# Performance work log

Hardware: AMD Instinct MI355X
Metric: run time of the kernel (lower is better)

## Reference

```python
import jax, jax.numpy as jnp
import numpy as np

N_HEAD = 16
N_KV = 4
HEAD_DIM = 128
EPS = float(np.finfo(np.float32).eps)  # torch F.rms_norm default eps


def _rope_tables(T, half, dtype=jnp.float32):
    inv_freq = 1.0 / (10000.0 ** (jnp.arange(half, dtype=dtype) / half))
    ang = jnp.arange(T, dtype=dtype)[:, None] * inv_freq[None, :]  # (T, half)
    cos = jnp.cos(ang)[None, :, None, :]  # (1, T, 1, half)
    sin = jnp.sin(ang)[None, :, None, :]
    return cos, sin


def setup_inputs() -> dict:
    key = jax.random.key(0)
    ks = jax.random.split(key, 5)
    B, T, C = 2, 2048, 2048
    x = jax.random.normal(ks[0], (B, T, C), dtype=jnp.float32)
    cos, sin = _rope_tables(T, HEAD_DIM // 2)
    s = 0.02
    W_Q = jax.random.normal(ks[1], (C, N_HEAD * HEAD_DIM), dtype=jnp.float32) * s
    W_K = jax.random.normal(ks[2], (C, N_KV * HEAD_DIM), dtype=jnp.float32) * s
    W_V = jax.random.normal(ks[3], (C, N_KV * HEAD_DIM), dtype=jnp.float32) * s
    W_O = jax.random.normal(ks[4], (C, C), dtype=jnp.float32) * s
    return {"x": x, "cos": cos, "sin": sin, "W_Q": W_Q, "W_K": W_K, "W_V": W_V, "W_O": W_O}


def _apply_rope(x, cos, sin):
    # x: (B,T,H,D); cos/sin: (1,T,1,D/2)
    d = x.shape[-1] // 2
    x1, x2 = x[..., :d], x[..., d:]
    return jnp.concatenate([x1 * cos + x2 * sin, -x1 * sin + x2 * cos], axis=-1)


def _rms_norm(x):
    return x * jax.lax.rsqrt(jnp.mean(x * x, axis=-1, keepdims=True) + EPS)


def reference(x, cos, sin, W_Q, W_K, W_V, W_O):
    B, T, C = x.shape
    G = N_HEAD // N_KV  # kv groups
    q = (x @ W_Q).reshape(B, T, N_HEAD, HEAD_DIM)
    k = (x @ W_K).reshape(B, T, N_KV, HEAD_DIM)
    v = (x @ W_V).reshape(B, T, N_KV, HEAD_DIM)
    q = _rms_norm(_apply_rope(q, cos[:, :T], sin[:, :T]))
    k = _rms_norm(_apply_rope(k, cos[:, :T], sin[:, :T]))
    # GQA: avoid materializing expanded K/V; group q by kv head
    qg = q.reshape(B, T, N_KV, G, HEAD_DIM)
    scale = 1.0 / jnp.sqrt(jnp.asarray(HEAD_DIM, dtype=x.dtype))
    scores = jnp.einsum("btkgd,bskd->bkgts", qg, k) * scale  # (B,Kv,G,T,T)
    causal = jnp.tril(jnp.ones((T, T), dtype=bool))
    scores = jnp.where(causal, scores, jnp.asarray(-jnp.inf, dtype=scores.dtype))
    attn = jax.nn.softmax(scores, axis=-1)
    out = jnp.einsum("bkgts,bskd->btkgd", attn, v).reshape(B, T, C)
    return out @ W_O
```

## Files before the change

kernel.cpp:

```cpp
#include <hip/hip_runtime.h>
#include <hip/hip_bf16.h>
#include <stdint.h>

typedef __bf16 bf16_4 __attribute__((ext_vector_type(4)));
typedef __bf16 bf16_8 __attribute__((ext_vector_type(8)));
typedef float f32x4 __attribute__((ext_vector_type(4)));

#define AS1 __attribute__((address_space(1)))
#define AS3 __attribute__((address_space(3)))

__device__ __forceinline__ void gload_lds16(const void* g, void* l) {
  __builtin_amdgcn_global_load_lds((const AS1 void*)g, (AS3 void*)l, 16, 0, 0);
}

__global__ void detect_dtype(const void* __restrict__ cosT, int* __restrict__ flag) {
  uint32_t w = *reinterpret_cast<const uint32_t*>(cosT);
  *flag = ((w & 0xFFFFu) == 0x3F80u) ? 1 : 0;
}

__global__ __launch_bounds__(256) void to_bf16_vec(const void* __restrict__ src,
                                                   __bf16* __restrict__ dst,
                                                   int n8, const int* __restrict__ flag) {
  const int i = blockIdx.x * 256 + threadIdx.x;
  if (i >= n8) return;
  if (*flag) {
    reinterpret_cast<int4*>(dst)[i] = reinterpret_cast<const int4*>(src)[i];
  } else {
    const float4* s = reinterpret_cast<const float4*>(src);
    const float4 a = s[2 * i], b = s[2 * i + 1];
    __bf16 o[8] = {(__bf16)a.x, (__bf16)a.y, (__bf16)a.z, (__bf16)a.w,
                   (__bf16)b.x, (__bf16)b.y, (__bf16)b.z, (__bf16)b.w};
    reinterpret_cast<int4*>(dst)[i] = *reinterpret_cast<int4*>(o);
  }
}

__global__ __launch_bounds__(256) void tables_to_f32(const void* __restrict__ c,
                                                     const void* __restrict__ s,
                                                     float* __restrict__ dst, int n,
                                                     const int* __restrict__ flag) {
  const int i = blockIdx.x * 256 + threadIdx.x;
  if (i >= n) return;
  if (*flag) {
    dst[i]     = (float)reinterpret_cast<const __bf16*>(c)[i];
    dst[n + i] = (float)reinterpret_cast<const __bf16*>(s)[i];
  } else {
    dst[i]     = reinterpret_cast<const float*>(c)[i];
    dst[n + i] = reinterpret_cast<const float*>(s)[i];
  }
}

__global__ void transpose_all(const void* __restrict__ WQ, const void* __restrict__ WK,
                              const void* __restrict__ WV, const void* __restrict__ WO,
                              __bf16* __restrict__ Wt, __bf16* __restrict__ WOt,
                              const int* __restrict__ flag) {
  __shared__ __bf16 t[32][33];
  const int bx = blockIdx.x;
  const void* src;
  __bf16* dst;
  int C, c0;
  if (bx < 64)      { src = WQ; dst = Wt;                          C = 2048; c0 = bx * 32; }
  else if (bx < 80) { src = WK; dst = Wt + (size_t)2048 * 2048;    C = 512;  c0 = (bx - 64) * 32; }
  else if (bx < 96) { src = WV; dst = Wt + (size_t)2560 * 2048;    C = 512;  c0 = (bx - 80) * 32; }
  else              { src = WO; dst = WOt;                         C = 2048; c0 = (bx - 96) * 32; }
  const int r0 = blockIdx.y * 32;
  const bool isb = (*flag != 0);
  #pragma unroll
  for (int i = 0; i < 32; i += 8) {
    const size_t idx = (size_t)(r0 + threadIdx.y + i) * C + c0 + threadIdx.x;
    t[threadIdx.y + i][threadIdx.x] =
        isb ? reinterpret_cast<const __bf16*>(src)[idx]
            : (__bf16)reinterpret_cast<const float*>(src)[idx];
  }
  __syncthreads();
  #pragma unroll
  for (int i = 0; i < 32; i += 8)
    dst[(size_t)(c0 + threadIdx.y + i) * 2048 + r0 + threadIdx.x] = t[threadIdx.x][threadIdx.y + i];
}

__global__ void vtrans(const __bf16* __restrict__ qkv, __bf16* __restrict__ vt) {
  __shared__ __bf16 t[32][33];
  const int b = blockIdx.z;
  const int t0 = blockIdx.x * 32, c0 = blockIdx.y * 32;
  #pragma unroll
  for (int i = 0; i < 32; i += 8)
    t[threadIdx.y + i][threadIdx.x] =
        qkv[(size_t)(b * 2048 + t0 + threadIdx.y + i) * 3072 + 2560 + c0 + threadIdx.x];
  __syncthreads();
  #pragma unroll
  for (int i = 0; i < 32; i += 8)
    vt[(size_t)(b * 512 + c0 + threadIdx.y + i) * 2048 + t0 + threadIdx.x] =
        t[threadIdx.x][threadIdx.y + i];
}

template <int DYN>
__global__ __launch_bounds__(512) void gemm8p(const __bf16* __restrict__ A,
                                              const __bf16* __restrict__ Bt,
                                              void* __restrict__ Cv,
                                              int M, int N, int K,
                                              const int* __restrict__ flag) {
  __shared__ __attribute__((aligned(16))) __bf16 As[2][128 * 64];
  __shared__ __attribute__((aligned(16))) __bf16 Bs[2][256 * 64];
  const int tid = threadIdx.x;
  const int lane = tid & 63, w = tid >> 6;
  const int wm = w >> 2, wn = w & 3;
  const int r = lane & 15, g = lane >> 4;
  const int bm = blockIdx.x * 128, bn = blockIdx.y * 256;
  const bool isb = DYN ? (*flag != 0) : true;
  const int NT = K >> 6;

  f32x4 acc[4][4] = {};

#define STA(kt, p, j)                                                              \
  {                                                                                \
    const int o_ = tid * 16 + (j) * 8192;                                          \
    const int row_ = o_ >> 7, blk_ = (o_ >> 4) & 7;                                \
    gload_lds16(A + (size_t)(bm + row_) * K + (kt) * 64 + ((blk_ ^ (row_ & 7)) << 3), \
                (char*)As[p] + o_);                                                \
  }
#define STB(kt, p, j)                                                              \
  {                                                                                \
    const int o_ = tid * 16 + (j) * 8192;                                          \
    const int rl_ = o_ >> 7, blk_ = (o_ >> 4) & 7;                                 \
    const int gr_ = ((rl_ >> 5) & 3) * 64 + ((rl_ >> 7) & 1) * 32 + (rl_ & 31);    \
    gload_lds16(Bt + (size_t)(bn + gr_) * K + (kt) * 64 + ((blk_ ^ (rl_ & 7)) << 3), \
                (char*)Bs[p] + o_);                                                \
  }

  STA(0, 0, 0); STA(0, 0, 1);
  STB(0, 0, 0); STB(0, 0, 1); STB(0, 0, 2); STB(0, 0, 3);
  asm volatile("s_waitcnt vmcnt(2)\ns_barrier" ::: "memory");

  for (int kt = 0; kt < NT; ++kt) {
    const int cur = kt & 1, nxt = cur ^ 1;
    const bool pf = (kt + 1 < NT);
    const char* Ac = (const char*)As[cur];
    const char* Bc = (const char*)Bs[cur];

    bf16_8 af[4][2], bf[2][2];
    #pragma unroll
    for (int m = 0; m < 4; ++m)
      #pragma unroll
      for (int kk = 0; kk < 2; ++kk) {
        const int row = wm * 64 + m * 16 + r;
        af[m][kk] = *reinterpret_cast<const bf16_8*>(
            Ac + row * 128 + (((kk * 4 + g) ^ (row & 7)) << 4));
      }
    #pragma unroll
    for (int n = 0; n < 2; ++n)
      #pragma unroll
      for (int kk = 0; kk < 2; ++kk) {
        const int rl = wn * 32 + n * 16 + r;
        bf[n][kk] = *reinterpret_cast<const bf16_8*>(
            Bc + rl * 128 + (((kk * 4 + g) ^ (rl & 7)) << 4));
      }
    if (pf) { STA(kt + 1, nxt, 0); STA(kt + 1, nxt, 1); STB(kt + 1, nxt, 0); }
    __builtin_amdgcn_s_barrier();
    __builtin_amdgcn_s_setprio(1);
    #pragma unroll
    for (int kk = 0; kk < 2; ++kk)
      #pragma unroll
      for (int m = 0; m < 4; ++m)
        #pragma unroll
        for (int n = 0; n < 2; ++n)
          acc[m][n] = __builtin_amdgcn_mfma_f32_16x16x32_bf16(af[m][kk], bf[n][kk], acc[m][n], 0, 0, 0);
    __builtin_amdgcn_s_setprio(0);
    if (pf) asm volatile("s_waitcnt vmcnt(3)\ns_barrier" ::: "memory");
    else    asm volatile("s_waitcnt vmcnt(0)\ns_barrier" ::: "memory");

    bf16_8 bg[2][2];
    #pragma unroll
    for (int n = 0; n < 2; ++n)
      #pragma unroll
      for (int kk = 0; kk < 2; ++kk) {
        const int rl = 128 + wn * 32 + n * 16 + r;
        bg[n][kk] = *reinterpret_cast<const bf16_8*>(
            Bc + rl * 128 + (((kk * 4 + g) ^ (rl & 7)) << 4));
      }
    if (pf) { STB(kt + 1, nxt, 1); STB(kt + 1, nxt, 2); STB(kt + 1, nxt, 3); }
    __builtin_amdgcn_s_barrier();
    __builtin_amdgcn_s_setprio(1);
    #pragma unroll
    for (int kk = 0; kk < 2; ++kk)
      #pragma unroll
      for (int m = 0; m < 4; ++m)
        #pragma unroll
        for (int n = 0; n < 2; ++n)
          acc[m][n + 2] = __builtin_amdgcn_mfma_f32_16x16x32_bf16(af[m][kk], bg[n][kk], acc[m][n + 2], 0, 0, 0);
    __builtin_amdgcn_s_setprio(0);
    if (pf) asm volatile("s_waitcnt vmcnt(2)\ns_barrier" ::: "memory");
    else    asm volatile("s_waitcnt vmcnt(0)\ns_barrier" ::: "memory");
  }
#undef STA
#undef STB

  #pragma unroll
  for (int m = 0; m < 4; ++m)
    #pragma unroll
    for (int n = 0; n < 4; ++n)
      #pragma unroll
      for (int j = 0; j < 4; ++j) {
        const int row = bm + wm * 64 + m * 16 + g * 4 + j;
        const int col = bn + wn * 64 + n * 16 + r;
        const float v = acc[m][n][j];
        if (isb) reinterpret_cast<__bf16*>(Cv)[(size_t)row * N + col] = (__bf16)v;
        else     reinterpret_cast<float*>(Cv)[(size_t)row * N + col] = v;
      }
}

__global__ __launch_bounds__(256) void rope_rms(__bf16* __restrict__ qkv,
                                                const float* __restrict__ csF) {
  const int gw = blockIdx.x * 4 + (threadIdx.x >> 6);
  const int lane = threadIdx.x & 63;
  const int head = gw % 20;
  const int m = gw / 20;
  const int t = m & 2047;
  __bf16* p = qkv + (size_t)m * 3072 + head * 128;
  const float x1 = (float)p[lane];
  const float x2 = (float)p[lane + 64];
  const float c = csF[t * 64 + lane];
  const float s = csF[131072 + t * 64 + lane];
  const float y1 = x1 * c + x2 * s;
  const float y2 = x2 * c - x1 * s;
  float ss = y1 * y1 + y2 * y2;
  #pragma unroll
  for (int mk = 32; mk >= 1; mk >>= 1) ss += __shfl_xor(ss, mk, 64);
  const float inv = rsqrtf(ss * (1.0f / 128.0f) + 1.1920929e-7f);
  p[lane] = (__bf16)(y1 * inv);
  p[lane + 64] = (__bf16)(y2 * inv);
}

__global__ __launch_bounds__(256) void attn_fwd3(const __bf16* __restrict__ qkv,
                                                 const __bf16* __restrict__ vt,
                                                 __bf16* __restrict__ out) {
  __shared__ __attribute__((aligned(16))) __bf16 Kl[2][64 * 128];
  __shared__ __attribute__((aligned(16))) __bf16 Vl[2][128 * 64];
  __shared__ __attribute__((aligned(16))) __bf16 Pl[4][16][72];

  const int tid = threadIdx.x, lane = tid & 63, w = tid >> 6;
  const int r = lane & 15, g = lane >> 4;
  const int lid = blockIdx.x;
  const int grp = lid & 7, inner = lid >> 3;
  const int b = grp >> 2, kvh = grp & 3;
  const int h = kvh * 4 + (inner & 3);
  const int xq = inner >> 2;
  const __bf16* Kbase = qkv + (size_t)(b * 2048) * 3072 + 2048 + kvh * 128;
  const __bf16* Vbase = vt + (size_t)((b * 4 + kvh) * 128) * 2048;
  const float sc2 = 0.08838834764831845f * 1.44269504f;

#define STAGE(kt, p)                                                            \
  {                                                                             \
    _Pragma("unroll")                                                           \
    for (int i_ = 0; i_ < 4; ++i_) {                                            \
      const int o_ = tid * 16 + i_ * 4096;                                      \
      const int krow_ = o_ >> 8;                                                \
      const int jj_ = (o_ >> 4) & 15;                                           \
      const int gj_ = (jj_ & 8) | ((jj_ ^ krow_) & 7);                          \
      gload_lds16(Kbase + (size_t)((kt) * 64 + krow_) * 3072 + gj_ * 8,         \
                  (char*)Kl[p] + o_);                                           \
      const int d_ = o_ >> 7;                                                   \
      const int j2_ = (o_ >> 4) & 7;                                            \
      const int g2_ = j2_ ^ (d_ & 7);                                           \
      gload_lds16(Vbase + (size_t)d_ * 2048 + (kt) * 64 + g2_ * 8,              \
                  (char*)Vl[p] + o_);                                           \
    }                                                                           \
  }

  for (int sidx = 0; sidx < 2; ++sidx) {
    const int qt = sidx ? (31 - xq) : xq;
    const int qrow0 = qt * 64 + w * 16;
    const int qpos = qrow0 + r;

    bf16_8 qf[4];
    {
      const __bf16* qp = qkv + (size_t)(b * 2048 + qrow0 + r) * 3072 + h * 128 + g * 8;
      #pragma unroll
      for (int kb = 0; kb < 4; ++kb) qf[kb] = *reinterpret_cast<const bf16_8*>(qp + kb * 32);
    }

    f32x4 accO[8] = {};
    float mst = -1e30f, lst = 0.0f;
    const int nt = qt + 1;

    STAGE(0, 0);
    asm volatile("s_waitcnt vmcnt(0)" ::: "memory");
    __syncthreads();

    for (int kt = 0; kt < nt; ++kt) {
      const int cur = kt & 1;
      if (kt + 1 < nt) STAGE(kt + 1, cur ^ 1);
      const char* Kc = (const char*)Kl[cur];
      const char* Vc = (const char*)Vl[cur];

      f32x4 sacc[4] = {};
      #pragma unroll
      for (int kb = 0; kb < 4; ++kb) {
        const int jj = kb * 4 + g;
        const int jp = (jj & 8) | ((jj ^ (r & 7)) & 7);
        #pragma unroll
        for (int n = 0; n < 4; ++n) {
          const bf16_8 kf = *reinterpret_cast<const bf16_8*>(Kc + (n * 16 + r) * 256 + jp * 16);
          sacc[n] = __builtin_amdgcn_mfma_f32_16x16x32_bf16(kf, qf[kb], sacc[n], 0, 0, 0);
        }
      }

      float p[4][4];
      float pm = -1e30f;
      #pragma unroll
      for (int n = 0; n < 4; ++n)
        #pragma unroll
        for (int j = 0; j < 4; ++j) {
          float s = sacc[n][j] * sc2;
          p[n][j] = s;
          pm = fmaxf(pm, s);
        }
      if (kt == qt) {
        pm = -1e30f;
        #pragma unroll
        for (int n = 0; n < 4; ++n)
          #pragma unroll
          for (int j = 0; j < 4; ++j) {
            if (kt * 64 + n * 16 + g * 4 + j > qpos) p[n][j] = -1e30f;
            pm = fmaxf(pm, p[n][j]);
          }
      }
      pm = fmaxf(pm, __shfl_xor(pm, 16, 64));
      pm = fmaxf(pm, __shfl_xor(pm, 32, 64));

      float mn;
      const bool defer = __all(pm - mst <= 12.0f);
      if (defer) {
        mn = mst;
      } else {
        mn = fmaxf(mst, pm);
        const float alpha = exp2f(mst - mn);
        mst = mn;
        lst *= alpha;
        float av[4];
        #pragma unroll
        for (int j = 0; j < 4; ++j) av[j] = __shfl(alpha, g * 4 + j, 64);
        #pragma unroll
        for (int dt = 0; dt < 8; ++dt)
          #pragma unroll
          for (int j = 0; j < 4; ++j) accO[dt][j] *= av[j];
      }
      float rs = 0.0f;
      #pragma unroll
      for (int n = 0; n < 4; ++n)
        #pragma unroll
        for (int j = 0; j < 4; ++j) {
          p[n][j] = exp2f(p[n][j] - mn);
          rs += p[n][j];
        }
      rs += __shfl_xor(rs, 16, 64);
      rs += __shfl_xor(rs, 32, 64);
      lst += rs;

      #pragma unroll
      for (int n = 0; n < 4; ++n) {
        bf16_4 pk;
        #pragma unroll
        for (int j = 0; j < 4; ++j) pk[j] = (__bf16)p[n][j];
        *reinterpret_cast<bf16_4*>(&Pl[w][r][n * 16 + g * 4]) = pk;
      }

      #pragma unroll
      for (int half = 0; half < 2; ++half) {
        const bf16_8 pa = *reinterpret_cast<const bf16_8*>(&Pl[w][r][half * 32 + g * 8]);
        #pragma unroll
        for (int dt = 0; dt < 8; ++dt) {
          const int d = dt * 16 + r;
          const bf16_8 vf = *reinterpret_cast<const bf16_8*>(Vc + d * 128 + ((half * 4 + g) ^ (d & 7)) * 16);
          accO[dt] = __builtin_amdgcn_mfma_f32_16x16x32_bf16(pa, vf, accO[dt], 0, 0, 0);
        }
      }

      asm volatile("s_waitcnt vmcnt(0)" ::: "memory");
      __syncthreads();
    }

    float lv[4];
    #pragma unroll
    for (int j = 0; j < 4; ++j) lv[j] = 1.0f / __shfl(lst, g * 4 + j, 64);
    #pragma unroll
    for (int dt = 0; dt < 8; ++dt)
      #pragma unroll
      for (int j = 0; j < 4; ++j) {
        const int t = qrow0 + g * 4 + j;
        out[(size_t)(b * 2048 + t) * 2048 + h * 128 + dt * 16 + r] = (__bf16)(accO[dt][j] * lv[j]);
      }
  }
#undef STAGE
}

extern "C" void kernel_launch(void* const* d_in, const int* in_sizes, int n_in,
                              void* d_out, int out_size, void* d_ws, size_t ws_size,
                              hipStream_t stream) {
  const void* x    = d_in[0];
  const void* cosT = d_in[1];
  const void* sinT = d_in[2];
  const void* W_Q  = d_in[3];
  const void* W_K  = d_in[4];
  const void* W_V  = d_in[5];
  const void* W_O  = d_in[6];

  const int B = 2, T = 2048, C = 2048;
  const int M = B * T;
  const int NQKV = 3072;

  char* ws = (char*)d_ws;
  int*    flag = (int*)ws;                       ws += 256;
  float*  csF  = (float*)ws;                     ws += (size_t)2 * 131072 * 4;
  __bf16* xb   = (__bf16*)ws;                    ws += (size_t)M * C * 2;
  __bf16* Wt   = (__bf16*)ws;                    ws += (size_t)NQKV * C * 2;
  __bf16* WOt  = (__bf16*)ws;                    ws += (size_t)C * C * 2;
  __bf16* QKV  = (__bf16*)ws;                    ws += (size_t)M * NQKV * 2;
  __bf16* AO   = (__bf16*)ws;                    ws += (size_t)M * C * 2;
  __bf16* VT   = xb;

  detect_dtype<<<1, 1, 0, stream>>>(cosT, flag);
  tables_to_f32<<<131072 / 256, 256, 0, stream>>>(cosT, sinT, csF, 131072, flag);
  to_bf16_vec<<<(M * C / 8) / 256, 256, 0, stream>>>(x, xb, M * C / 8, flag);

  transpose_all<<<dim3(160, 64), dim3(32, 8), 0, stream>>>(W_Q, W_K, W_V, W_O, Wt, WOt, flag);

  gemm8p<0><<<dim3(M / 128, NQKV / 256), 512, 0, stream>>>(xb, Wt, QKV, M, NQKV, C, flag);
  rope_rms<<<dim3(M * 20 / 4), 256, 0, stream>>>(QKV, csF);
  vtrans<<<dim3(T / 32, 512 / 32, B), dim3(32, 8), 0, stream>>>(QKV, VT);
  attn_fwd3<<<dim3(512), 256, 0, stream>>>(QKV, VT, AO);
  gemm8p<1><<<dim3(M / 128, C / 256), 512, 0, stream>>>(AO, WOt, d_out, M, C, C, flag);
}
```

Measured before the change: 231.7 us.

## Process paired causal query tiles in one shared KV loop in attention

After: 230.0 us. No clear change (-0.7%).

```diff
diff --git a/kernel.cpp b/kernel.cpp
--- a/kernel.cpp
+++ b/kernel.cpp
@@ -229,7 +229,7 @@
   p[lane + 64] = (__bf16)(y2 * inv);
 }
 
-__global__ __launch_bounds__(256) void attn_fwd3(const __bf16* __restrict__ qkv,
+__global__ __launch_bounds__(256) void attn_fwd4(const __bf16* __restrict__ qkv,
                                                  const __bf16* __restrict__ vt,
                                                  __bf16* __restrict__ out) {
   __shared__ __attribute__((aligned(16))) __bf16 Kl[2][64 * 128];
@@ -242,7 +242,9 @@
   const int grp = lid & 7, inner = lid >> 3;
   const int b = grp >> 2, kvh = grp & 3;
   const int h = kvh * 4 + (inner & 3);
-  const int xq = inner >> 2;
+  const int x = inner >> 2;
+  const int qtA = x, qtB = 31 - x;
+  const int nA = qtA + 1, nB = qtB + 1;
   const __bf16* Kbase = qkv + (size_t)(b * 2048) * 3072 + 2048 + kvh * 128;
   const __bf16* Vbase = vt + (size_t)((b * 4 + kvh) * 128) * 2048;
   const float sc2 = 0.08838834764831845f * 1.44269504f;
@@ -265,131 +267,143 @@
     }                                                                           \
   }
 
-  for (int sidx = 0; sidx < 2; ++sidx) {
-    const int qt = sidx ? (31 - xq) : xq;
-    const int qrow0 = qt * 64 + w * 16;
-    const int qpos = qrow0 + r;
-
-    bf16_8 qf[4];
-    {
-      const __bf16* qp = qkv + (size_t)(b * 2048 + qrow0 + r) * 3072 + h * 128 + g * 8;
-      #pragma unroll
-      for (int kb = 0; kb < 4; ++kb) qf[kb] = *reinterpret_cast<const bf16_8*>(qp + kb * 32);
+#define TILE(qt_, qf_, acc_, mst_, lst_)                                        \
+  do {                                                                          \
+    f32x4 sacc[4] = {};                                                         \
+    _Pragma("unroll")                                                           \
+    for (int kb = 0; kb < 4; ++kb) {                                            \
+      const int jj = kb * 4 + g;                                                \
+      const int jp = (jj & 8) | ((jj ^ (r & 7)) & 7);                           \
+      _Pragma("unroll")                                                         \
+      for (int n = 0; n < 4; ++n) {                                             \
+        const bf16_8 kf = *reinterpret_cast<const bf16_8*>(Kc + (n * 16 + r) * 256 + jp * 16); \
+        sacc[n] = __builtin_amdgcn_mfma_f32_16x16x32_bf16(kf, qf_[kb], sacc[n], 0, 0, 0); \
+      }                                                                         \
+    }                                                                           \
+    float p[4][4];                                                              \
+    float pm = -1e30f;                                                          \
+    _Pragma("unroll")                                                           \
+    for (int n = 0; n < 4; ++n)                                                 \
+      _Pragma("unroll")                                                         \
+      for (int j = 0; j < 4; ++j) {                                             \
+        float s = sacc[n][j] * sc2;                                             \
+        p[n][j] = s;                                                            \
+        pm = fmaxf(pm, s);                                                      \
+      }                                                                         \
+    if (kt == (qt_)) {                                                          \
+      const int qpos_ = (qt_) * 64 + w * 16 + r;                                \
+      pm = -1e30f;                                                              \
+      _Pragma("unroll")                                                         \
+      for (int n = 0; n < 4; ++n)                                               \
+        _Pragma("unroll")                                                       \
+        for (int j = 0; j < 4; ++j) {                                           \
+          if (kt * 64 + n * 16 + g * 4 + j > qpos_) p[n][j] = -1e30f;           \
+          pm = fmaxf(pm, p[n][j]);                                              \
+        }                                                                       \
+    }                                                                           \
+    pm = fmaxf(pm, __shfl_xor(pm, 16, 64));                                     \
+    pm = fmaxf(pm, __shfl_xor(pm, 32, 64));                                     \
+    float mn = mst_;                                                            \
+    if (!__all(pm - mst_ <= 12.0f)) {                                           \
+      mn = fmaxf(mst_, pm);                                                     \
+      const float alpha = exp2f(mst_ - mn);                                     \
+      mst_ = mn;                                                                \
+      lst_ *= alpha;                                                            \
+      float av[4];                                                              \
+      _Pragma("unroll")                                                         \
+      for (int j = 0; j < 4; ++j) av[j] = __shfl(alpha, g * 4 + j, 64);         \
+      _Pragma("unroll")                                                         \
+      for (int dt = 0; dt < 8; ++dt)                                            \
+        _Pragma("unroll")                                                       \
+        for (int j = 0; j < 4; ++j) acc_[dt][j] *= av[j];                       \
+    }                                                                           \
+    float rs = 0.0f;                                                            \
+    _Pragma("unroll")                                                           \
+    for (int n = 0; n < 4; ++n)                                                 \
+      _Pragma("unroll")                                                         \
+      for (int j = 0; j < 4; ++j) {                                             \
+        p[n][j] = exp2f(p[n][j] - mn);                                          \
+        rs += p[n][j];                                                          \
+      }                                                                         \
+    rs += __shfl_xor(rs, 16, 64);                                               \
+    rs += __shfl_xor(rs, 32, 64);                                               \
+    lst_ += rs;                                                                 \
+    _Pragma("unroll")                                                           \
+    for (int n = 0; n < 4; ++n) {                                               \
+      bf16_4 pk;                                                                \
+      _Pragma("unroll")                                                         \
+      for (int j = 0; j < 4; ++j) pk[j] = (__bf16)p[n][j];                      \
+      *reinterpret_cast<bf16_4*>(&Pl[w][r][n * 16 + g * 4]) = pk;               \
+    }                                                                           \
+    _Pragma("unroll")                                                           \
+    for (int half = 0; half < 2; ++half) {                                      \
+      const bf16_8 pa = *reinterpret_cast<const bf16_8*>(&Pl[w][r][half * 32 + g * 8]); \
+      _Pragma("unroll")                                                         \
+      for (int dt = 0; dt < 8; ++dt) {                                          \
+        const int d = dt * 16 + r;                                              \
+        const bf16_8 vf = *reinterpret_cast<const bf16_8*>(Vc + d * 128 + ((half * 4 + g) ^ (d & 7)) * 16); \
+        acc_[dt] = __builtin_amdgcn_mfma_f32_16x16x32_bf16(pa, vf, acc_[dt], 0, 0, 0); \
+      }                                                                         \
+    }                                                                           \
+  } while (0)
+
+  bf16_8 qfA[4], qfB[4];
+  {
+    const __bf16* qpA = qkv + (size_t)(b * 2048 + qtA * 64 + w * 16 + r) * 3072 + h * 128 + g * 8;
+    const __bf16* qpB = qkv + (size_t)(b * 2048 + qtB * 64 + w * 16 + r) * 3072 + h * 128 + g * 8;
+    #pragma unroll
+    for (int kb = 0; kb < 4; ++kb) {
+      qfA[kb] = *reinterpret_cast<const bf16_8*>(qpA + kb * 32);
+      qfB[kb] = *reinterpret_cast<const bf16_8*>(qpB + kb * 32);
     }
-
-    f32x4 accO[8] = {};
-    float mst = -1e30f, lst = 0.0f;
-    const int nt = qt + 1;
-
-    STAGE(0, 0);
+  }
+
+  f32x4 accA[8] = {}, accB[8] = {};
+  float mstA = -1e30f, lstA = 0.0f, mstB = -1e30f, lstB = 0.0f;
+
+  STAGE(0, 0);
+  asm volatile("s_waitcnt vmcnt(0)" ::: "memory");
+  __syncthreads();
+
+  for (int kt = 0; kt < nB; ++kt) {
+    const int cur = kt & 1;
+    if (kt + 1 < nB) STAGE(kt + 1, cur ^ 1);
+    const char* Kc = (const char*)Kl[cur];
+    const char* Vc = (const char*)Vl[cur];
+
+    if (kt < nA) TILE(qtA, qfA, accA, mstA, lstA);
+    TILE(qtB, qfB, accB, mstB, lstB);
+
     asm volatile("s_waitcnt vmcnt(0)" ::: "memory");
     __syncthreads();
-
-    for (int kt = 0; kt < nt; ++kt) {
-      const int cur = kt & 1;
-      if (kt + 1 < nt) STAGE(kt + 1, cur ^ 1);
-      const char* Kc = (const char*)Kl[cur];
-      const char* Vc = (const char*)Vl[cur];
-
-      f32x4 sacc[4] = {};
-      #pragma unroll
-      for (int kb = 0; kb < 4; ++kb) {
-        const int jj = kb * 4 + g;
-        const int jp = (jj & 8) | ((jj ^ (r & 7)) & 7);
-        #pragma unroll
-        for (int n = 0; n < 4; ++n) {
-          const bf16_8 kf = *reinterpret_cast<const bf16_8*>(Kc + (n * 16 + r) * 256 + jp * 16);
-          sacc[n] = __builtin_amdgcn_mfma_f32_16x16x32_bf16(kf, qf[kb], sacc[n], 0, 0, 0);
-        }
-      }
-
-      float p[4][4];
-      float pm = -1e30f;
-      #pragma unroll
-      for (int n = 0; n < 4; ++n)
-        #pragma unroll
-        for (int j = 0; j < 4; ++j) {
-          float s = sacc[n][j] * sc2;
-          p[n][j] = s;
-          pm = fmaxf(pm, s);
-        }
-      if (kt == qt) {
-        pm = -1e30f;
-        #pragma unroll
-        for (int n = 0; n < 4; ++n)
-          #pragma unroll
-          for (int j = 0; j < 4; ++j) {
-            if (kt * 64 + n * 16 + g * 4 + j > qpos) p[n][j] = -1e30f;
-            pm = fmaxf(pm, p[n][j]);
-          }
-      }
-      pm = fmaxf(pm, __shfl_xor(pm, 16, 64));
-      pm = fmaxf(pm, __shfl_xor(pm, 32, 64));
-
-      float mn;
-      const bool defer = __all(pm - mst <= 12.0f);
-      if (defer) {
-        mn = mst;
-      } else {
-        mn = fmaxf(mst, pm);
-        const float alpha = exp2f(mst - mn);
-        mst = mn;
-        lst *= alpha;
-        float av[4];
-        #pragma unroll
-        for (int j = 0; j < 4; ++j) av[j] = __shfl(alpha, g * 4 + j, 64);
-        #pragma unroll
-        for (int dt = 0; dt < 8; ++dt)
-          #pragma unroll
-          for (int j = 0; j < 4; ++j) accO[dt][j] *= av[j];
-      }
-      float rs = 0.0f;
-      #pragma unroll
-      for (int n = 0; n < 4; ++n)
-        #pragma unroll
-        for (int j = 0; j < 4; ++j) {
-          p[n][j] = exp2f(p[n][j] - mn);
-          rs += p[n][j];
-        }
-      rs += __shfl_xor(rs, 16, 64);
-      rs += __shfl_xor(rs, 32, 64);
-      lst += rs;
-
-      #pragma unroll
-      for (int n = 0; n < 4; ++n) {
-        bf16_4 pk;
-        #pragma unroll
-        for (int j = 0; j < 4; ++j) pk[j] = (__bf16)p[n][j];
-        *reinterpret_cast<bf16_4*>(&Pl[w][r][n * 16 + g * 4]) = pk;
-      }
-
-      #pragma unroll
-      for (int half = 0; half < 2; ++half) {
-        const bf16_8 pa = *reinterpret_cast<const bf16_8*>(&Pl[w][r][half * 32 + g * 8]);
-        #pragma unroll
-        for (int dt = 0; dt < 8; ++dt) {
-          const int d = dt * 16 + r;
-          const bf16_8 vf = *reinterpret_cast<const bf16_8*>(Vc + d * 128 + ((half * 4 + g) ^ (d & 7)) * 16);
-          accO[dt] = __builtin_amdgcn_mfma_f32_16x16x32_bf16(pa, vf, accO[dt], 0, 0, 0);
-        }
-      }
-
-      asm volatile("s_waitcnt vmcnt(0)" ::: "memory");
-      __syncthreads();
-    }
-
+  }
+
+  {
     float lv[4];
     #pragma unroll
-    for (int j = 0; j < 4; ++j) lv[j] = 1.0f / __shfl(lst, g * 4 + j, 64);
+    for (int j = 0; j < 4; ++j) lv[j] = 1.0f / __shfl(lstA, g * 4 + j, 64);
     #pragma unroll
     for (int dt = 0; dt < 8; ++dt)
       #pragma unroll
       for (int j = 0; j < 4; ++j) {
-        const int t = qrow0 + g * 4 + j;
-        out[(size_t)(b * 2048 + t) * 2048 + h * 128 + dt * 16 + r] = (__bf16)(accO[dt][j] * lv[j]);
+        const int t = qtA * 64 + w * 16 + g * 4 + j;
+        out[(size_t)(b * 2048 + t) * 2048 + h * 128 + dt * 16 + r] = (__bf16)(accA[dt][j] * lv[j]);
+      }
+  }
+  {
+    float lv[4];
+    #pragma unroll
+    for (int j = 0; j < 4; ++j) lv[j] = 1.0f / __shfl(lstB, g * 4 + j, 64);
+    #pragma unroll
+    for (int dt = 0; dt < 8; ++dt)
+      #pragma unroll
+      for (int j = 0; j < 4; ++j) {
+        const int t = qtB * 64 + w * 16 + g * 4 + j;
+        out[(size_t)(b * 2048 + t) * 2048 + h * 128 + dt * 16 + r] = (__bf16)(accB[dt][j] * lv[j]);
       }
   }
 #undef STAGE
+#undef TILE
 }
 
 extern "C" void kernel_launch(void* const* d_in, const int* in_sizes, int n_in,
@@ -426,6 +440,6 @@
   gemm8p<0><<<dim3(M / 128, NQKV / 256), 512, 0, stream>>>(xb, Wt, QKV, M, NQKV, C, flag);
   rope_rms<<<dim3(M * 20 / 4), 256, 0, stream>>>(QKV, csF);
   vtrans<<<dim3(T / 32, 512 / 32, B), dim3(32, 8), 0, stream>>>(QKV, VT);
-  attn_fwd3<<<dim3(512), 256, 0, stream>>>(QKV, VT, AO);
+  attn_fwd4<<<dim3(512), 256, 0, stream>>>(QKV, VT, AO);
   gemm8p<1><<<dim3(M / 128, C / 256), 512, 0, stream>>>(AO, WOt, d_out, M, C, C, flag);
 }
```

## Split attention into one q-tile per block, single-buffer K/V, fold scale into Q

Applied to the files above, without the earlier changes.

Measured after the change: 227.9 us. Within noise of the previous version (-1.6%).

```diff
diff --git a/kernel.cpp b/kernel.cpp
--- a/kernel.cpp
+++ b/kernel.cpp
@@ -224,17 +224,18 @@
   float ss = y1 * y1 + y2 * y2;
   #pragma unroll
   for (int mk = 32; mk >= 1; mk >>= 1) ss += __shfl_xor(ss, mk, 64);
-  const float inv = rsqrtf(ss * (1.0f / 128.0f) + 1.1920929e-7f);
+  float inv = rsqrtf(ss * (1.0f / 128.0f) + 1.1920929e-7f);
+  if (head < 16) inv *= 0.12751743f;
   p[lane] = (__bf16)(y1 * inv);
   p[lane + 64] = (__bf16)(y2 * inv);
 }
 
-__global__ __launch_bounds__(256) void attn_fwd3(const __bf16* __restrict__ qkv,
+__global__ __launch_bounds__(256) void attn_fwd7(const __bf16* __restrict__ qkv,
                                                  const __bf16* __restrict__ vt,
                                                  __bf16* __restrict__ out) {
-  __shared__ __attribute__((aligned(16))) __bf16 Kl[2][64 * 128];
-  __shared__ __attribute__((aligned(16))) __bf16 Vl[2][128 * 64];
-  __shared__ __attribute__((aligned(16))) __bf16 Pl[4][16][72];
+  __shared__ __attribute__((aligned(16))) __bf16 Kl[64 * 128];
+  __shared__ __attribute__((aligned(16))) __bf16 Vl[128 * 64];
+  __shared__ __attribute__((aligned(16))) __bf16 Pl[4][16][64];
 
   const int tid = threadIdx.x, lane = tid & 63, w = tid >> 6;
   const int r = lane & 15, g = lane >> 4;
@@ -242,12 +243,12 @@
   const int grp = lid & 7, inner = lid >> 3;
   const int b = grp >> 2, kvh = grp & 3;
   const int h = kvh * 4 + (inner & 3);
-  const int xq = inner >> 2;
+  const int qt = 31 - (inner >> 2);
+  const int nt = qt + 1;
   const __bf16* Kbase = qkv + (size_t)(b * 2048) * 3072 + 2048 + kvh * 128;
   const __bf16* Vbase = vt + (size_t)((b * 4 + kvh) * 128) * 2048;
-  const float sc2 = 0.08838834764831845f * 1.44269504f;
-
-#define STAGE(kt, p)                                                            \
+
+#define STAGE(kt)                                                               \
   {                                                                             \
     _Pragma("unroll")                                                           \
     for (int i_ = 0; i_ < 4; ++i_) {                                            \
@@ -256,139 +257,127 @@
       const int jj_ = (o_ >> 4) & 15;                                           \
       const int gj_ = (jj_ & 8) | ((jj_ ^ krow_) & 7);                          \
       gload_lds16(Kbase + (size_t)((kt) * 64 + krow_) * 3072 + gj_ * 8,         \
-                  (char*)Kl[p] + o_);                                           \
+                  (char*)Kl + o_);                                              \
       const int d_ = o_ >> 7;                                                   \
       const int j2_ = (o_ >> 4) & 7;                                            \
       const int g2_ = j2_ ^ (d_ & 7);                                           \
       gload_lds16(Vbase + (size_t)d_ * 2048 + (kt) * 64 + g2_ * 8,              \
-                  (char*)Vl[p] + o_);                                           \
+                  (char*)Vl + o_);                                              \
     }                                                                           \
   }
 
-  for (int sidx = 0; sidx < 2; ++sidx) {
-    const int qt = sidx ? (31 - xq) : xq;
-    const int qrow0 = qt * 64 + w * 16;
-    const int qpos = qrow0 + r;
-
-    bf16_8 qf[4];
-    {
-      const __bf16* qp = qkv + (size_t)(b * 2048 + qrow0 + r) * 3072 + h * 128 + g * 8;
-      #pragma unroll
-      for (int kb = 0; kb < 4; ++kb) qf[kb] = *reinterpret_cast<const bf16_8*>(qp + kb * 32);
-    }
-
-    f32x4 accO[8] = {};
-    float mst = -1e30f, lst = 0.0f;
-    const int nt = qt + 1;
-
-    STAGE(0, 0);
+  bf16_8 qf[4];
+  {
+    const __bf16* qp = qkv + (size_t)(b * 2048 + qt * 64 + w * 16 + r) * 3072 + h * 128 + g * 8;
+    #pragma unroll
+    for (int kb = 0; kb < 4; ++kb) qf[kb] = *reinterpret_cast<const bf16_8*>(qp + kb * 32);
+  }
+
+  char* const plw = (char*)Pl + w * 2048;
+  f32x4 accO[8] = {};
+  float mst = -1e30f, lst = 0.0f;
+
+  for (int kt = 0; kt < nt; ++kt) {
+    STAGE(kt);
     asm volatile("s_waitcnt vmcnt(0)" ::: "memory");
     __syncthreads();
 
-    for (int kt = 0; kt < nt; ++kt) {
-      const int cur = kt & 1;
-      if (kt + 1 < nt) STAGE(kt + 1, cur ^ 1);
-      const char* Kc = (const char*)Kl[cur];
-      const char* Vc = (const char*)Vl[cur];
-
-      f32x4 sacc[4] = {};
-      #pragma unroll
-      for (int kb = 0; kb < 4; ++kb) {
-        const int jj = kb * 4 + g;
-        const int jp = (jj & 8) | ((jj ^ (r & 7)) & 7);
-        #pragma unroll
-        for (int n = 0; n < 4; ++n) {
-          const bf16_8 kf = *reinterpret_cast<const bf16_8*>(Kc + (n * 16 + r) * 256 + jp * 16);
-          sacc[n] = __builtin_amdgcn_mfma_f32_16x16x32_bf16(kf, qf[kb], sacc[n], 0, 0, 0);
-        }
-      }
-
-      float p[4][4];
-      float pm = -1e30f;
+    f32x4 sacc[4] = {};
+    #pragma unroll
+    for (int kb = 0; kb < 4; ++kb) {
+      const int jj = kb * 4 + g;
+      const int jp = (jj & 8) | ((jj ^ (r & 7)) & 7);
+      #pragma unroll
+      for (int n = 0; n < 4; ++n) {
+        const bf16_8 kf = *reinterpret_cast<const bf16_8*>((char*)Kl + (n * 16 + r) * 256 + jp * 16);
+        sacc[n] = __builtin_amdgcn_mfma_f32_16x16x32_bf16(kf, qf[kb], sacc[n], 0, 0, 0);
+      }
+    }
+
+    float p[4][4];
+    float pm = -1e30f;
+    #pragma unroll
+    for (int n = 0; n < 4; ++n)
+      #pragma unroll
+      for (int j = 0; j < 4; ++j) {
+        p[n][j] = sacc[n][j];
+        pm = fmaxf(pm, p[n][j]);
+      }
+    if (kt == qt) {
+      const int qpos = qt * 64 + w * 16 + r;
+      pm = -1e30f;
       #pragma unroll
       for (int n = 0; n < 4; ++n)
         #pragma unroll
         for (int j = 0; j < 4; ++j) {
-          float s = sacc[n][j] * sc2;
-          p[n][j] = s;
-          pm = fmaxf(pm, s);
+          if (kt * 64 + n * 16 + g * 4 + j > qpos) p[n][j] = -1e30f;
+          pm = fmaxf(pm, p[n][j]);
         }
-      if (kt == qt) {
-        pm = -1e30f;
+    }
+    pm = fmaxf(pm, __shfl_xor(pm, 16, 64));
+    pm = fmaxf(pm, __shfl_xor(pm, 32, 64));
+
+    float mn = mst;
+    if (!__all(pm - mst <= 12.0f)) {
+      mn = fmaxf(mst, pm);
+      const float alpha = exp2f(mst - mn);
+      mst = mn;
+      lst *= alpha;
+      float av[4];
+      #pragma unroll
+      for (int j = 0; j < 4; ++j) av[j] = __shfl(alpha, g * 4 + j, 64);
+      #pragma unroll
+      for (int dt = 0; dt < 8; ++dt)
         #pragma unroll
-        for (int n = 0; n < 4; ++n)
-          #pragma unroll
-          for (int j = 0; j < 4; ++j) {
-            if (kt * 64 + n * 16 + g * 4 + j > qpos) p[n][j] = -1e30f;
-            pm = fmaxf(pm, p[n][j]);
-          }
-      }
-      pm = fmaxf(pm, __shfl_xor(pm, 16, 64));
-      pm = fmaxf(pm, __shfl_xor(pm, 32, 64));
-
-      float mn;
-      const bool defer = __all(pm - mst <= 12.0f);
-      if (defer) {
-        mn = mst;
-      } else {
-        mn = fmaxf(mst, pm);
-        const float alpha = exp2f(mst - mn);
-        mst = mn;
-        lst *= alpha;
-        float av[4];
-        #pragma unroll
-        for (int j = 0; j < 4; ++j) av[j] = __shfl(alpha, g * 4 + j, 64);
-        #pragma unroll
-        for (int dt = 0; dt < 8; ++dt)
-          #pragma unroll
-          for (int j = 0; j < 4; ++j) accO[dt][j] *= av[j];
-      }
-      float rs = 0.0f;
-      #pragma unroll
-      for (int n = 0; n < 4; ++n)
-        #pragma unroll
-        for (int j = 0; j < 4; ++j) {
-          p[n][j] = exp2f(p[n][j] - mn);
-          rs += p[n][j];
-        }
-      rs += __shfl_xor(rs, 16, 64);
-      rs += __shfl_xor(rs, 32, 64);
-      lst += rs;
-
-      #pragma unroll
-      for (int n = 0; n < 4; ++n) {
-        bf16_4 pk;
-        #pragma unroll
-        for (int j = 0; j < 4; ++j) pk[j] = (__bf16)p[n][j];
-        *reinterpret_cast<bf16_4*>(&Pl[w][r][n * 16 + g * 4]) = pk;
-      }
-
-      #pragma unroll
-      for (int half = 0; half < 2; ++half) {
-        const bf16_8 pa = *reinterpret_cast<const bf16_8*>(&Pl[w][r][half * 32 + g * 8]);
-        #pragma unroll
-        for (int dt = 0; dt < 8; ++dt) {
-          const int d = dt * 16 + r;
-          const bf16_8 vf = *reinterpret_cast<const bf16_8*>(Vc + d * 128 + ((half * 4 + g) ^ (d & 7)) * 16);
-          accO[dt] = __builtin_amdgcn_mfma_f32_16x16x32_bf16(pa, vf, accO[dt], 0, 0, 0);
-        }
-      }
-
-      asm volatile("s_waitcnt vmcnt(0)" ::: "memory");
-      __syncthreads();
-    }
-
-    float lv[4];
-    #pragma unroll
-    for (int j = 0; j < 4; ++j) lv[j] = 1.0f / __shfl(lst, g * 4 + j, 64);
-    #pragma unroll
-    for (int dt = 0; dt < 8; ++dt)
+        for (int j = 0; j < 4; ++j) accO[dt][j] *= av[j];
+    }
+    float rs = 0.0f;
+    #pragma unroll
+    for (int n = 0; n < 4; ++n)
       #pragma unroll
       for (int j = 0; j < 4; ++j) {
-        const int t = qrow0 + g * 4 + j;
-        out[(size_t)(b * 2048 + t) * 2048 + h * 128 + dt * 16 + r] = (__bf16)(accO[dt][j] * lv[j]);
-      }
-  }
+        p[n][j] = exp2f(p[n][j] - mn);
+        rs += p[n][j];
+      }
+    rs += __shfl_xor(rs, 16, 64);
+    rs += __shfl_xor(rs, 32, 64);
+    lst += rs;
+
+    #pragma unroll
+    for (int n = 0; n < 4; ++n) {
+      bf16_4 pk;
+      #pragma unroll
+      for (int j = 0; j < 4; ++j) pk[j] = (__bf16)p[n][j];
+      const int blk = 2 * n + (g >> 1);
+      char* pw = plw + r * 128 + ((blk ^ (r & 7)) << 4) + (g & 1) * 8;
+      *reinterpret_cast<bf16_4*>(pw) = pk;
+    }
+
+    #pragma unroll
+    for (int half = 0; half < 2; ++half) {
+      const bf16_8 pa = *reinterpret_cast<const bf16_8*>(
+          plw + r * 128 + (((half * 4 + g) ^ (r & 7)) << 4));
+      #pragma unroll
+      for (int dt = 0; dt < 8; ++dt) {
+        const int d = dt * 16 + r;
+        const bf16_8 vf = *reinterpret_cast<const bf16_8*>((char*)Vl + d * 128 + ((half * 4 + g) ^ (d & 7)) * 16);
+        accO[dt] = __builtin_amdgcn_mfma_f32_16x16x32_bf16(pa, vf, accO[dt], 0, 0, 0);
+      }
+    }
+
+    __syncthreads();
+  }
+
+  float lv[4];
+  #pragma unroll
+  for (int j = 0; j < 4; ++j) lv[j] = 1.0f / __shfl(lst, g * 4 + j, 64);
+  #pragma unroll
+  for (int dt = 0; dt < 8; ++dt)
+    #pragma unroll
+    for (int j = 0; j < 4; ++j) {
+      const int t = qt * 64 + w * 16 + g * 4 + j;
+      out[(size_t)(b * 2048 + t) * 2048 + h * 128 + dt * 16 + r] = (__bf16)(accO[dt][j] * lv[j]);
+    }
 #undef STAGE
 }
 
@@ -426,6 +415,6 @@
   gemm8p<0><<<dim3(M / 128, NQKV / 256), 512, 0, stream>>>(xb, Wt, QKV, M, NQKV, C, flag);
   rope_rms<<<dim3(M * 20 / 4), 256, 0, stream>>>(QKV, csF);
   vtrans<<<dim3(T / 32, 512 / 32, B), dim3(32, 8), 0, stream>>>(QKV, VT);
-  attn_fwd3<<<dim3(512), 256, 0, stream>>>(QKV, VT, AO);
+  attn_fwd7<<<dim3(1024), 256, 0, stream>>>(QKV, VT, AO);
   gemm8p<1><<<dim3(M / 128, C / 256), 512, 0, stream>>>(AO, WOt, d_out, M, C, C, flag);
 }
```
